# Performance work log

Hardware: AMD Instinct MI355X
Metric: run time of the kernel (lower is better)

Reference implementation:

```python
import jax, jax.numpy as jnp
import numpy as np

B, S, J, D, H = 8, 256, 24, 128, 8
DEPTH = D // H  # 16


def _pos_encoding(seq_len, d_model):
    # matches position_encoding: angle = pos / 10000^(2*(i//2)/d_model);
    # even dims -> sin, odd dims -> cos. shape (1, seq_len, 1, d_model)
    pos = jnp.arange(seq_len, dtype=jnp.float32)[:, None]
    i = jnp.arange(d_model)
    rates = 1.0 / jnp.power(10000.0, (2 * (i // 2)).astype(jnp.float32) / d_model)
    ang = pos * rates[None, :]
    pe = jnp.where(i % 2 == 0, jnp.sin(ang), jnp.cos(ang))
    return pe[None, :, None, :]


def setup_inputs() -> dict:
    key = jax.random.key(0)
    ks = jax.random.split(key, 10)
    std = float(np.sqrt(1.0 / np.sqrt(D * D)))  # matches initialize()
    x = jax.random.normal(ks[0], (B, S, J, D), jnp.float32)
    # look-ahead mask on the (S-1, S-1) sub-block: 1 = masked (future)
    mask = jnp.triu(jnp.ones((S - 1, S - 1), jnp.float32), k=1)
    Wq = jax.random.normal(ks[1], (D, D), jnp.float32) * std
    bq = jnp.zeros((D,), jnp.float32)
    Wk = jax.random.normal(ks[2], (D, D), jnp.float32) * std
    bk = jnp.zeros((D,), jnp.float32)
    Wv = jax.random.normal(ks[3], (D, D), jnp.float32) * std
    bv = jnp.zeros((D,), jnp.float32)
    Wo = jax.random.normal(ks[4], (D, D), jnp.float32) * std
    bo = jnp.zeros((D,), jnp.float32)
    return {"x": x, "mask": mask, "Wq": Wq, "bq": bq, "Wk": Wk, "bk": bk,
            "Wv": Wv, "bv": bv, "Wo": Wo, "bo": bo}


def _split_heads(t):
    # (B, S, J, D) -> (B, J, H, S, DEPTH)
    b, s, j, d = t.shape
    t = t.transpose(0, 2, 1, 3)                 # (B, J, S, D)
    t = t.reshape(b, j, s, H, DEPTH)            # (B, J, S, H, DEPTH)
    return t.transpose(0, 1, 3, 2, 4)           # (B, J, H, S, DEPTH)


def reference(x, mask, Wq, bq, Wk, bk, Wv, bv, Wo, bo):
    b, s, j, d = x.shape
    x = x + _pos_encoding(S, D)[:, :s]          # broadcast over batch & joints
    # shared QKV projections (same math as linear applied on (J,B,S,D))
    q = _split_heads(jnp.einsum('bsjd,de->bsje', x, Wq) + bq)
    k = _split_heads(jnp.einsum('bsjd,de->bsje', x, Wk) + bk)
    v = _split_heads(jnp.einsum('bsjd,de->bsje', x, Wv) + bv)
    scores = jnp.einsum('bjhqd,bjhkd->bjhqk', q, k) / jnp.sqrt(
        jnp.asarray(DEPTH, x.dtype))            # (B, J, H, S, S)
    # custom partial-block masking: only the [1:, 1:] sub-block is masked
    scores = scores.at[:, :, :, 1:, 1:].add(mask * -1e9)
    w = jax.nn.softmax(scores, axis=-1)
    out = jnp.einsum('bjhqk,bjhkd->bjhqd', w, v)  # (B, J, H, S, DEPTH)
    out = out.transpose(0, 3, 1, 2, 4).reshape(b, s, j, d)
    out = jnp.einsum('bsjd,de->bsje', out, Wo) + bo
    return (out, mask)
```

## Files before the change

kernel.cpp:

```cpp
#include <hip/hip_runtime.h>
#include <hip/hip_bf16.h>
#include <math.h>

#define NB 8
#define NS 256
#define NJ 24
#define ND 128
#define NH 8
#define NDEP 16
#define NROW (NB * NS * NJ)

typedef unsigned short u16;
typedef unsigned int u32;
typedef float f32x4 __attribute__((ext_vector_type(4)));
typedef short bf16x8 __attribute__((ext_vector_type(8)));
typedef unsigned short us8 __attribute__((ext_vector_type(8)));
typedef unsigned short us4 __attribute__((ext_vector_type(4)));

#define MFMA16(a, b, c) __builtin_amdgcn_mfma_f32_16x16x32_bf16(a, b, c, 0, 0, 0)

#define QSCALE 0.36067376022224085f

__device__ __forceinline__ u16 f2bf(float f) {
    union { __hip_bfloat16 h; u16 u; } cv;
    cv.h = __float2bfloat16(f);
    return cv.u;
}
__device__ __forceinline__ u32 pack2bf(float a, float b) {
    return (u32)f2bf(a) | ((u32)f2bf(b) << 16);
}

__global__ __launch_bounds__(256) void prep_kernel(
        const float* __restrict__ Wq, const float* __restrict__ Wk,
        const float* __restrict__ Wv, const float* __restrict__ Wo,
        const float* __restrict__ mask,
        float* __restrict__ pe, u16* __restrict__ wt,
        float* __restrict__ mask_dst) {
    int idx = blockIdx.x * 256 + threadIdx.x;
    if (idx < 32768) {
        int s = idx >> 7, d = idx & 127;
        float r = __expf(-(float)(d & ~1) * (9.210340371976184f / 128.0f));
        float ang = (float)s * r;
        pe[idx] = (d & 1) ? cosf(ang) : sinf(ang);
    } else if (idx < 98304) {
        int e = idx - 32768;
        int w = e >> 14, rr = e & 16383;
        int n = rr >> 7, kk = rr & 127;
        const float* W = (w == 0) ? Wq : (w == 1) ? Wk : (w == 2) ? Wv : Wo;
        float val = W[kk * 128 + n];
        if (w == 0) val *= QSCALE;
        wt[e] = f2bf(val);
    } else {
        int e = idx - 98304;
        if (e < (NS - 1) * (NS - 1)) mask_dst[e] = mask[e];
    }
}

__global__ __launch_bounds__(256) void qkv_kernel(
        const float* __restrict__ x, const float* __restrict__ pe,
        const u16* __restrict__ wt,
        const float* __restrict__ bq, const float* __restrict__ bk,
        const float* __restrict__ bv,
        u16* __restrict__ qo, u16* __restrict__ ko, u16* __restrict__ vo) {
    __shared__ u16 xs[64][136];
    __shared__ u16 wsh[128][136];
    const int t = threadIdx.x;
    const int row0 = blockIdx.x * 64;

#pragma unroll
    for (int i = 0; i < 8; i++) {
        int f4 = t + i * 256;
        int r = f4 >> 5, c4 = (f4 & 31) * 4;
        int grow = row0 + r;
        int s = (grow / NJ) & (NS - 1);
        float4 xv = *(const float4*)&x[(size_t)grow * ND + c4];
        float4 pv = *(const float4*)&pe[s * ND + c4];
        us4 b4;
        b4[0] = f2bf(xv.x + pv.x); b4[1] = f2bf(xv.y + pv.y);
        b4[2] = f2bf(xv.z + pv.z); b4[3] = f2bf(xv.w + pv.w);
        *(us4*)&xs[r][c4] = b4;
    }

    const int l = t & 63, wv = t >> 6, gg = l >> 4, c = l & 15;
    const float* bm[3] = {bq, bk, bv};
    u16* om[3] = {qo, ko, vo};

#pragma unroll
    for (int w = 0; w < 3; w++) {
        __syncthreads();
#pragma unroll
        for (int i = 0; i < 8; i++) {
            int u8 = t + i * 256;
            int r = u8 >> 4, c8 = (u8 & 15) * 8;
            *(us8*)&wsh[r][c8] = *(const us8*)&wt[w * 16384 + r * 128 + c8];
        }
        __syncthreads();
        f32x4 acc[8] = {};
#pragma unroll
        for (int ks = 0; ks < 4; ks++) {
            bf16x8 af = *(const bf16x8*)&xs[wv * 16 + c][ks * 32 + gg * 8];
#pragma unroll
            for (int nf = 0; nf < 8; nf++) {
                bf16x8 bf_ = *(const bf16x8*)&wsh[nf * 16 + c][ks * 32 + gg * 8];
                acc[nf] = MFMA16(af, bf_, acc[nf]);
            }
        }
        __syncthreads();
        const float bscale = (w == 0) ? QSCALE : 1.0f;
#pragma unroll
        for (int nf = 0; nf < 8; nf++) {
            float bb = bm[w][nf * 16 + c] * bscale;
#pragma unroll
            for (int r = 0; r < 4; r++)
                wsh[wv * 16 + gg * 4 + r][nf * 16 + c] = f2bf(acc[nf][r] + bb);
        }
        __syncthreads();
#pragma unroll
        for (int i = 0; i < 4; i++) {
            int u8 = t + i * 256;
            int row = u8 >> 4, piece = u8 & 15;
            int grow = row0 + row;
            int b = grow / 6144, rem = grow % 6144;
            int s = rem / NJ, jj = rem % NJ;
            int hh = piece >> 1, half = piece & 1;
            us8 val = *(const us8*)&wsh[row][piece * 8];
            *(us8*)&om[w][(size_t)((b * NJ + jj) * NH + hh) * 4096 + s * 16 +
                          half * 8] = val;
        }
    }
}

__global__ __launch_bounds__(512) void attn_kernel(
        const u16* __restrict__ q, const u16* __restrict__ k,
        const u16* __restrict__ v, u16* __restrict__ o) {
    __shared__ u16 ksh[256][24];
    __shared__ uint4 vts4[16][32];

    const int t = threadIdx.x;
    const int bjh = blockIdx.x;
    const size_t base = (size_t)bjh * 4096;

    {
        int row = t >> 1, c8 = (t & 1) * 8;
        *(us8*)&ksh[row][c8] = *(const us8*)&k[base + row * 16 + c8];
    }
    {
        int r = t >> 1, h8 = (t & 1) * 8;
        us8 vv = *(const us8*)&v[base + r * 16 + h8];
        int slot = (r & 0xE0) | ((r & 12) << 1) | ((r & 16) >> 2) | (r & 3);
        int cell = slot >> 3, e = slot & 7;
#pragma unroll
        for (int dd = 0; dd < 8; dd++) {
            int d = h8 + dd;
            ((u16*)&vts4[d][cell ^ (d & 7)])[e] = vv[dd];
        }
    }
    __syncthreads();

    const int wv = t >> 6, l = t & 63, gg = l >> 4, c = l & 15;
    const int h = bjh & 7, j = (bjh >> 3) % NJ, b = bjh / (NJ * NH);
    const size_t obase = (size_t)b * 786432 + (size_t)j * 128 + h * 16 + c;

#pragma unroll
    for (int slot = 0; slot < 2; slot++) {
        const int g = wv + slot * 8;
        const int dchk = g >> 2;
        const int qrow = 16 * g + c;
        const int thr = (qrow == 0) ? 0x7fffffff : qrow;

        bf16x8 bq_ = {};
        if (gg < 2)
            bq_ = *(const bf16x8*)&q[base + (size_t)qrow * 16 + gg * 8];

        f32x4 oa = {};
        float ls = 0.0f;
#pragma unroll
        for (int ch = 0; ch < 4; ch++) {
            const bool domask = (g == 0) || (ch >= dchk);
            const int thr2 = domask ? thr : 0x7fffffff;
            f32x4 st[4];
#pragma unroll
            for (int kf = 0; kf < 4; kf++) {
                bf16x8 ak = {};
                if (gg < 2)
                    ak = *(const bf16x8*)&ksh[ch * 64 + kf * 16 + c][gg * 8];
                f32x4 zz = {};
                st[kf] = MFMA16(ak, bq_, zz);
            }
            uint2 pk[4];
#pragma unroll
            for (int kf = 0; kf < 4; kf++) {
#pragma unroll
                for (int r = 0; r < 4; r++) {
                    int key = ch * 64 + kf * 16 + gg * 4 + r;
                    float vv = (key > thr2) ? -1.0e9f : st[kf][r];
                    float p = __builtin_amdgcn_exp2f(vv);
                    st[kf][r] = p;
                    ls += p;
                }
                pk[kf].x = pack2bf(st[kf][0], st[kf][1]);
                pk[kf].y = pack2bf(st[kf][2], st[kf][3]);
            }
            uint4 a0 = make_uint4(pk[0].x, pk[0].y, pk[1].x, pk[1].y);
            uint4 a1 = make_uint4(pk[2].x, pk[2].y, pk[3].x, pk[3].y);
#pragma unroll
            for (int ks = 0; ks < 2; ks++) {
                bf16x8 ap = __builtin_bit_cast(bf16x8, ks ? a1 : a0);
                uint4 vb4 = vts4[c][(ch * 8 + ks * 4 + gg) ^ (c & 7)];
                bf16x8 bv_ = __builtin_bit_cast(bf16x8, vb4);
                oa = MFMA16(ap, bv_, oa);
            }
        }
        ls += __shfl_xor(ls, 16);
        ls += __shfl_xor(ls, 32);
        const float inv = 1.0f / ls;
#pragma unroll
        for (int r = 0; r < 4; r++) {
            float ir = __shfl(inv, gg * 4 + r);
            int s = 16 * g + gg * 4 + r;
            o[obase + (size_t)s * 3072] = f2bf(oa[r] * ir);
        }
    }
}

__global__ __launch_bounds__(256) void proj_kernel(
        const u16* __restrict__ in, const u16* __restrict__ wt,
        const float* __restrict__ bias, float* __restrict__ out) {
    __shared__ u16 xs[64][136];
    __shared__ u16 wsh[128][136];
    const int t = threadIdx.x;
    const int row0 = blockIdx.x * 64;
#pragma unroll
    for (int i = 0; i < 4; i++) {
        int u8 = t + i * 256;
        int r = u8 >> 4, c8 = (u8 & 15) * 8;
        *(us8*)&xs[r][c8] = *(const us8*)&in[(size_t)(row0 + r) * ND + c8];
    }
#pragma unroll
    for (int i = 0; i < 8; i++) {
        int u8 = t + i * 256;
        int r = u8 >> 4, c8 = (u8 & 15) * 8;
        *(us8*)&wsh[r][c8] = *(const us8*)&wt[r * 128 + c8];
    }
    __syncthreads();
    const int l = t & 63, wv = t >> 6, gg = l >> 4, c = l & 15;
    f32x4 acc[8] = {};
#pragma unroll
    for (int ks = 0; ks < 4; ks++) {
        bf16x8 af = *(const bf16x8*)&xs[wv * 16 + c][ks * 32 + gg * 8];
#pragma unroll
        for (int nf = 0; nf < 8; nf++) {
            bf16x8 bf_ = *(const bf16x8*)&wsh[nf * 16 + c][ks * 32 + gg * 8];
            acc[nf] = MFMA16(af, bf_, acc[nf]);
        }
    }
    __syncthreads();
    float* bounce = (float*)&wsh[0][0];
#pragma unroll
    for (int nf = 0; nf < 8; nf++) {
        float bb = bias[nf * 16 + c];
#pragma unroll
        for (int r = 0; r < 4; r++)
            bounce[(wv * 16 + gg * 4 + r) * 132 + nf * 16 + c] = acc[nf][r] + bb;
    }
    __syncthreads();
#pragma unroll
    for (int i = 0; i < 8; i++) {
        int idx = t + i * 256;
        int row = idx >> 5, p4 = idx & 31;
        float4 vv = *(const float4*)&bounce[row * 132 + p4 * 4];
        *(float4*)&out[(size_t)(row0 + row) * 128 + p4 * 4] = vv;
    }
}

extern "C" void kernel_launch(void* const* d_in, const int* in_sizes, int n_in,
                              void* d_out, int out_size, void* d_ws, size_t ws_size,
                              hipStream_t stream) {
    const float* x    = (const float*)d_in[0];
    const float* mask = (const float*)d_in[1];
    const float* Wq   = (const float*)d_in[2];
    const float* bq   = (const float*)d_in[3];
    const float* Wk   = (const float*)d_in[4];
    const float* bk   = (const float*)d_in[5];
    const float* Wv   = (const float*)d_in[6];
    const float* bv   = (const float*)d_in[7];
    const float* Wo   = (const float*)d_in[8];
    const float* bo   = (const float*)d_in[9];
    float* out = (float*)d_out;

    char* ws = (char*)d_ws;
    float* pe = (float*)ws;
    u16* wt  = (u16*)(ws + 131072);
    u16* qb  = (u16*)(ws + 262144);
    u16* kb  = qb + (size_t)NROW * ND;
    u16* vb  = kb + (size_t)NROW * ND;
    u16* ab  = vb + (size_t)NROW * ND;

    prep_kernel<<<639, 256, 0, stream>>>(Wq, Wk, Wv, Wo, mask, pe, wt,
                                         out + (size_t)NROW * ND);
    qkv_kernel<<<NROW / 64, 256, 0, stream>>>(x, pe, wt, bq, bk, bv, qb, kb, vb);
    attn_kernel<<<NB * NJ * NH, 512, 0, stream>>>(qb, kb, vb, ab);
    proj_kernel<<<NROW / 64, 256, 0, stream>>>(ab, wt + 3 * 16384, bo, out);
}
```

Baseline: 67.41 us.

## Skip fully-masked key chunks, balance causal work across waves, use packed bf16 convert

The attention kernel now skips key chunks lying entirely above the causal diagonal instead of computing them and masking to -1e9. Query groups are assigned to waves through a lookup table so each wave gets a balanced mix of short and long rows. The mask comparison is applied only on diagonal chunks, bf16 packing uses the hardware v_cvt_pk_bf16_f32 instruction, and MFMA sections are wrapped in s_setprio to favor matrix issue. The risk is added divergence in control flow, and the inline asm may round differently from the previous conversion.

```diff
diff --git a/kernel.cpp b/kernel.cpp
--- a/kernel.cpp
+++ b/kernel.cpp
@@ -26,8 +26,10 @@
     cv.h = __float2bfloat16(f);
     return cv.u;
 }
-__device__ __forceinline__ u32 pack2bf(float a, float b) {
-    return (u32)f2bf(a) | ((u32)f2bf(b) << 16);
+__device__ __forceinline__ u32 cvtpk(float lo, float hi) {
+    u32 r;
+    asm("v_cvt_pk_bf16_f32 %0, %1, %2" : "=v"(r) : "v"(lo), "v"(hi));
+    return r;
 }
 
 __global__ __launch_bounds__(256) void prep_kernel(
@@ -160,11 +162,13 @@
     const int wv = t >> 6, l = t & 63, gg = l >> 4, c = l & 15;
     const int h = bjh & 7, j = (bjh >> 3) % NJ, b = bjh / (NJ * NH);
     const size_t obase = (size_t)b * 786432 + (size_t)j * 128 + h * 16 + c;
+    const unsigned long long TBL = 0xBA79685F4E3D2C10ull;
 
 #pragma unroll
     for (int slot = 0; slot < 2; slot++) {
-        const int g = wv + slot * 8;
+        const int g = (int)((TBL >> ((wv * 2 + slot) * 4)) & 15);
         const int dchk = g >> 2;
+        const int nch = (g == 0) ? 4 : dchk + 1;
         const int qrow = 16 * g + c;
         const int thr = (qrow == 0) ? 0x7fffffff : qrow;
 
@@ -176,9 +180,10 @@
         float ls = 0.0f;
 #pragma unroll
         for (int ch = 0; ch < 4; ch++) {
-            const bool domask = (g == 0) || (ch >= dchk);
-            const int thr2 = domask ? thr : 0x7fffffff;
+            if (ch >= nch) continue;
+            const bool diag = (g == 0) || (ch == dchk);
             f32x4 st[4];
+            __builtin_amdgcn_s_setprio(1);
 #pragma unroll
             for (int kf = 0; kf < 4; kf++) {
                 bf16x8 ak = {};
@@ -187,22 +192,38 @@
                 f32x4 zz = {};
                 st[kf] = MFMA16(ak, bq_, zz);
             }
-            uint2 pk[4];
-#pragma unroll
-            for (int kf = 0; kf < 4; kf++) {
-#pragma unroll
-                for (int r = 0; r < 4; r++) {
-                    int key = ch * 64 + kf * 16 + gg * 4 + r;
-                    float vv = (key > thr2) ? -1.0e9f : st[kf][r];
-                    float p = __builtin_amdgcn_exp2f(vv);
-                    st[kf][r] = p;
-                    ls += p;
+            __builtin_amdgcn_s_setprio(0);
+            u32 pw[8];
+            if (diag) {
+#pragma unroll
+                for (int kf = 0; kf < 4; kf++) {
+#pragma unroll
+                    for (int r = 0; r < 4; r++) {
+                        int key = ch * 64 + kf * 16 + gg * 4 + r;
+                        float vv = (key > thr) ? -1.0e9f : st[kf][r];
+                        float p = __builtin_amdgcn_exp2f(vv);
+                        st[kf][r] = p;
+                        ls += p;
+                    }
+                    pw[kf * 2]     = cvtpk(st[kf][0], st[kf][1]);
+                    pw[kf * 2 + 1] = cvtpk(st[kf][2], st[kf][3]);
                 }
-                pk[kf].x = pack2bf(st[kf][0], st[kf][1]);
-                pk[kf].y = pack2bf(st[kf][2], st[kf][3]);
+            } else {
+#pragma unroll
+                for (int kf = 0; kf < 4; kf++) {
+#pragma unroll
+                    for (int r = 0; r < 4; r++) {
+                        float p = __builtin_amdgcn_exp2f(st[kf][r]);
+                        st[kf][r] = p;
+                        ls += p;
+                    }
+                    pw[kf * 2]     = cvtpk(st[kf][0], st[kf][1]);
+                    pw[kf * 2 + 1] = cvtpk(st[kf][2], st[kf][3]);
+                }
             }
-            uint4 a0 = make_uint4(pk[0].x, pk[0].y, pk[1].x, pk[1].y);
-            uint4 a1 = make_uint4(pk[2].x, pk[2].y, pk[3].x, pk[3].y);
+            uint4 a0 = make_uint4(pw[0], pw[1], pw[2], pw[3]);
+            uint4 a1 = make_uint4(pw[4], pw[5], pw[6], pw[7]);
+            __builtin_amdgcn_s_setprio(1);
 #pragma unroll
             for (int ks = 0; ks < 2; ks++) {
                 bf16x8 ap = __builtin_bit_cast(bf16x8, ks ? a1 : a0);
@@ -210,6 +231,7 @@
                 bf16x8 bv_ = __builtin_bit_cast(bf16x8, vb4);
                 oa = MFMA16(ap, bv_, oa);
             }
+            __builtin_amdgcn_s_setprio(0);
         }
         ls += __shfl_xor(ls, 16);
         ls += __shfl_xor(ls, 32);
```

Result: faster. 57.53 us (-14.7%).

## Skip fully masked key chunks and pair query tiles per wave in attention

Applied to the files above, without the earlier changes.

The attention kernel now runs with 4 waves per block, and each wave handles two adjacent 16-row query tiles at once. The tiles are assigned through a lookup table so that causal work is balanced across waves, and the key-chunk loop stops after the last chunk that can contain unmasked keys, skipping fully masked chunks. K fragments and V loads are shared between the two tiles, and bf16 packing uses the hardware v_cvt_pk_bf16_f32 instruction. Risks are fewer waves per block, more registers per wave, and a data-dependent loop count; the skip relies on exp2 of -1e9 being exactly zero.

```diff
diff --git a/kernel.cpp b/kernel.cpp
--- a/kernel.cpp
+++ b/kernel.cpp
@@ -26,8 +26,10 @@
     cv.h = __float2bfloat16(f);
     return cv.u;
 }
-__device__ __forceinline__ u32 pack2bf(float a, float b) {
-    return (u32)f2bf(a) | ((u32)f2bf(b) << 16);
+__device__ __forceinline__ u32 cvtpk(float lo, float hi) {
+    u32 r;
+    asm("v_cvt_pk_bf16_f32 %0, %1, %2" : "=v"(r) : "v"(lo), "v"(hi));
+    return r;
 }
 
 __global__ __launch_bounds__(256) void prep_kernel(
@@ -130,7 +132,7 @@
     }
 }
 
-__global__ __launch_bounds__(512) void attn_kernel(
+__global__ __launch_bounds__(256) void attn_kernel(
         const u16* __restrict__ q, const u16* __restrict__ k,
         const u16* __restrict__ v, u16* __restrict__ o) {
     __shared__ u16 ksh[256][24];
@@ -140,12 +142,16 @@
     const int bjh = blockIdx.x;
     const size_t base = (size_t)bjh * 4096;
 
-    {
-        int row = t >> 1, c8 = (t & 1) * 8;
+#pragma unroll
+    for (int i = 0; i < 2; i++) {
+        int idx = t + i * 256;
+        int row = idx >> 1, c8 = (idx & 1) * 8;
         *(us8*)&ksh[row][c8] = *(const us8*)&k[base + row * 16 + c8];
     }
-    {
-        int r = t >> 1, h8 = (t & 1) * 8;
+#pragma unroll
+    for (int i = 0; i < 2; i++) {
+        int idx = t + i * 256;
+        int r = idx >> 1, h8 = (idx & 1) * 8;
         us8 vv = *(const us8*)&v[base + r * 16 + h8];
         int slot = (r & 0xE0) | ((r & 12) << 1) | ((r & 16) >> 2) | (r & 3);
         int cell = slot >> 3, e = slot & 7;
@@ -160,65 +166,97 @@
     const int wv = t >> 6, l = t & 63, gg = l >> 4, c = l & 15;
     const int h = bjh & 7, j = (bjh >> 3) % NJ, b = bjh / (NJ * NH);
     const size_t obase = (size_t)b * 786432 + (size_t)j * 128 + h * 16 + c;
-
-#pragma unroll
-    for (int slot = 0; slot < 2; slot++) {
-        const int g = wv + slot * 8;
-        const int dchk = g >> 2;
-        const int qrow = 16 * g + c;
-        const int thr = (qrow == 0) ? 0x7fffffff : qrow;
-
-        bf16x8 bq_ = {};
-        if (gg < 2)
-            bq_ = *(const bf16x8*)&q[base + (size_t)qrow * 16 + gg * 8];
-
-        f32x4 oa = {};
-        float ls = 0.0f;
-#pragma unroll
-        for (int ch = 0; ch < 4; ch++) {
-            const bool domask = (g == 0) || (ch >= dchk);
-            const int thr2 = domask ? thr : 0x7fffffff;
-            f32x4 st[4];
-#pragma unroll
-            for (int kf = 0; kf < 4; kf++) {
-                bf16x8 ak = {};
-                if (gg < 2)
-                    ak = *(const bf16x8*)&ksh[ch * 64 + kf * 16 + c][gg * 8];
-                f32x4 zz = {};
-                st[kf] = MFMA16(ak, bq_, zz);
+    const u32 TBL32 = 0xA86E4C20u;
+
+#pragma unroll
+    for (int phase = 0; phase < 2; phase++) {
+        const int gA = (int)((TBL32 >> ((wv * 2 + phase) * 4)) & 15);
+        const int gB = gA + 1;
+        const int nit = (gA == 0) ? 4 : (gB >> 2) + 1;
+        const int dchkA = gA >> 2, dchkB = gB >> 2;
+        const int qrowA = 16 * gA + c, qrowB = 16 * gB + c;
+        const int thrA = (qrowA == 0) ? 0x7fffffff : qrowA;
+        const int thrB = qrowB;
+
+        bf16x8 bqA = {}, bqB = {};
+        if (gg < 2) {
+            bqA = *(const bf16x8*)&q[base + (size_t)qrowA * 16 + gg * 8];
+            bqB = *(const bf16x8*)&q[base + (size_t)qrowB * 16 + gg * 8];
+        }
+
+        f32x4 oaA = {}, oaB = {};
+        float lsA = 0.0f, lsB = 0.0f;
+        for (int ch = 0; ch < nit; ++ch) {
+            const int tA = ((gA == 0) || (ch >= dchkA)) ? thrA : 0x7fffffff;
+            const int tB = (ch >= dchkB) ? thrB : 0x7fffffff;
+
+            bf16x8 ak0 = {}, ak1 = {}, ak2 = {}, ak3 = {};
+            if (gg < 2) {
+                ak0 = *(const bf16x8*)&ksh[ch * 64 + 0 * 16 + c][gg * 8];
+                ak1 = *(const bf16x8*)&ksh[ch * 64 + 1 * 16 + c][gg * 8];
+                ak2 = *(const bf16x8*)&ksh[ch * 64 + 2 * 16 + c][gg * 8];
+                ak3 = *(const bf16x8*)&ksh[ch * 64 + 3 * 16 + c][gg * 8];
             }
-            uint2 pk[4];
+            f32x4 zz = {};
+            f32x4 stA[4], stB[4];
+            stA[0] = MFMA16(ak0, bqA, zz);
+            stB[0] = MFMA16(ak0, bqB, zz);
+            stA[1] = MFMA16(ak1, bqA, zz);
+            stB[1] = MFMA16(ak1, bqB, zz);
+            stA[2] = MFMA16(ak2, bqA, zz);
+            stB[2] = MFMA16(ak2, bqB, zz);
+            stA[3] = MFMA16(ak3, bqA, zz);
+            stB[3] = MFMA16(ak3, bqB, zz);
+
+            u32 pwA[8], pwB[8];
 #pragma unroll
             for (int kf = 0; kf < 4; kf++) {
 #pragma unroll
                 for (int r = 0; r < 4; r++) {
                     int key = ch * 64 + kf * 16 + gg * 4 + r;
-                    float vv = (key > thr2) ? -1.0e9f : st[kf][r];
-                    float p = __builtin_amdgcn_exp2f(vv);
-                    st[kf][r] = p;
-                    ls += p;
+                    float sA = (key > tA) ? -1.0e9f : stA[kf][r];
+                    float sB = (key > tB) ? -1.0e9f : stB[kf][r];
+                    float pA = __builtin_amdgcn_exp2f(sA);
+                    float pB = __builtin_amdgcn_exp2f(sB);
+                    stA[kf][r] = pA;
+                    stB[kf][r] = pB;
+                    lsA += pA;
+                    lsB += pB;
                 }
-                pk[kf].x = pack2bf(st[kf][0], st[kf][1]);
-                pk[kf].y = pack2bf(st[kf][2], st[kf][3]);
+                pwA[kf * 2]     = cvtpk(stA[kf][0], stA[kf][1]);
+                pwA[kf * 2 + 1] = cvtpk(stA[kf][2], stA[kf][3]);
+                pwB[kf * 2]     = cvtpk(stB[kf][0], stB[kf][1]);
+                pwB[kf * 2 + 1] = cvtpk(stB[kf][2], stB[kf][3]);
             }
-            uint4 a0 = make_uint4(pk[0].x, pk[0].y, pk[1].x, pk[1].y);
-            uint4 a1 = make_uint4(pk[2].x, pk[2].y, pk[3].x, pk[3].y);
-#pragma unroll
-            for (int ks = 0; ks < 2; ks++) {
-                bf16x8 ap = __builtin_bit_cast(bf16x8, ks ? a1 : a0);
-                uint4 vb4 = vts4[c][(ch * 8 + ks * 4 + gg) ^ (c & 7)];
-                bf16x8 bv_ = __builtin_bit_cast(bf16x8, vb4);
-                oa = MFMA16(ap, bv_, oa);
-            }
-        }
-        ls += __shfl_xor(ls, 16);
-        ls += __shfl_xor(ls, 32);
-        const float inv = 1.0f / ls;
+            uint4 a0A = make_uint4(pwA[0], pwA[1], pwA[2], pwA[3]);
+            uint4 a1A = make_uint4(pwA[4], pwA[5], pwA[6], pwA[7]);
+            uint4 a0B = make_uint4(pwB[0], pwB[1], pwB[2], pwB[3]);
+            uint4 a1B = make_uint4(pwB[4], pwB[5], pwB[6], pwB[7]);
+            uint4 vb0 = vts4[c][(ch * 8 + 0 * 4 + gg) ^ (c & 7)];
+            uint4 vb1 = vts4[c][(ch * 8 + 1 * 4 + gg) ^ (c & 7)];
+            oaA = MFMA16(__builtin_bit_cast(bf16x8, a0A),
+                         __builtin_bit_cast(bf16x8, vb0), oaA);
+            oaB = MFMA16(__builtin_bit_cast(bf16x8, a0B),
+                         __builtin_bit_cast(bf16x8, vb0), oaB);
+            oaA = MFMA16(__builtin_bit_cast(bf16x8, a1A),
+                         __builtin_bit_cast(bf16x8, vb1), oaA);
+            oaB = MFMA16(__builtin_bit_cast(bf16x8, a1B),
+                         __builtin_bit_cast(bf16x8, vb1), oaB);
+        }
+        lsA += __shfl_xor(lsA, 16);
+        lsA += __shfl_xor(lsA, 32);
+        lsB += __shfl_xor(lsB, 16);
+        lsB += __shfl_xor(lsB, 32);
+        const float invA = 1.0f / lsA;
+        const float invB = 1.0f / lsB;
 #pragma unroll
         for (int r = 0; r < 4; r++) {
-            float ir = __shfl(inv, gg * 4 + r);
-            int s = 16 * g + gg * 4 + r;
-            o[obase + (size_t)s * 3072] = f2bf(oa[r] * ir);
+            float irA = __shfl(invA, gg * 4 + r);
+            float irB = __shfl(invB, gg * 4 + r);
+            int sA = 16 * gA + gg * 4 + r;
+            int sB = 16 * gB + gg * 4 + r;
+            o[obase + (size_t)sA * 3072] = f2bf(oaA[r] * irA);
+            o[obase + (size_t)sB * 3072] = f2bf(oaB[r] * irB);
         }
     }
 }
@@ -299,6 +337,6 @@
     prep_kernel<<<639, 256, 0, stream>>>(Wq, Wk, Wv, Wo, mask, pe, wt,
                                          out + (size_t)NROW * ND);
     qkv_kernel<<<NROW / 64, 256, 0, stream>>>(x, pe, wt, bq, bk, bv, qb, kb, vb);
-    attn_kernel<<<NB * NJ * NH, 512, 0, stream>>>(qb, kb, vb, ab);
+    attn_kernel<<<NB * NJ * NH, 256, 0, stream>>>(qb, kb, vb, ab);
     proj_kernel<<<NROW / 64, 256, 0, stream>>>(ab, wt + 3 * 16384, bo, out);
 }
```

Measured after the change: 60.44 us. -10.3%, faster.
